# Kernel optimization log

Hardware: AMD Instinct MI355X
Metric: run time of the kernel (lower is better)

## Reference

```python
import jax, jax.numpy as jnp
import numpy as np

N_PIX = 65536
RPT = 16
N_ENT = N_PIX * RPT
DIMS = 128
N_HEADS = 8
LN_EPS = 1e-6


def setup_inputs() -> dict:
    key = jax.random.key(0)
    ks = jax.random.split(key, 12)
    s = 1.0 / np.sqrt(DIMS)
    token = jax.random.normal(ks[0], (N_PIX, DIMS), dtype=jnp.float32)
    ctx = jax.random.normal(ks[1], (N_ENT, DIMS), dtype=jnp.float32)
    segms = jnp.repeat(jnp.arange(N_PIX, dtype=jnp.int32), RPT)  # sorted segment ids
    rpts = jnp.full((N_PIX,), RPT, dtype=jnp.int32)  # sums to N_ENT
    entry_mask = jax.random.bernoulli(ks[2], 0.9, (N_ENT,))
    return {
        "token": token,
        "ctx": ctx,
        "segms": segms,
        "rpts": rpts,
        "entry_mask": entry_mask,
        "Wq": jax.random.normal(ks[3], (DIMS, DIMS), jnp.float32) * s,
        "bq": jnp.zeros((DIMS,), jnp.float32),
        "Wk": jax.random.normal(ks[4], (DIMS, DIMS), jnp.float32) * s,
        "bk": jnp.zeros((DIMS,), jnp.float32),
        "Wv": jax.random.normal(ks[5], (DIMS, DIMS), jnp.float32) * s,
        "bv": jnp.zeros((DIMS,), jnp.float32),
        "Wo": jax.random.normal(ks[6], (DIMS, DIMS), jnp.float32) * s,
        "bo": jnp.zeros((DIMS,), jnp.float32),
        "ln_scale": jnp.ones((DIMS,), jnp.float32),
        "ln_bias": jnp.zeros((DIMS,), jnp.float32),
    }


def reference(token, ctx, segms, rpts, entry_mask,
              Wq, bq, Wk, bk, Wv, bv, Wo, bo, ln_scale, ln_bias):
    EPS = jnp.finfo(jnp.float32).eps
    n_entries = ctx.shape[0]
    n_pixels = token.shape[0]
    dims = ctx.shape[-1]
    hd = dims // N_HEADS  # head dim

    # query per pixel, expanded to entries via ragged repeat
    q = token @ Wq + bq                                          # [P, D]
    q = jnp.repeat(q, rpts, axis=0, total_repeat_length=n_entries)
    q = q.reshape(n_entries, N_HEADS, hd) / jnp.sqrt(jnp.float32(hd))
    k = (ctx @ Wk + bk).reshape(n_entries, N_HEADS, hd)
    v = (ctx @ Wv + bv).reshape(n_entries, N_HEADS, hd)

    w = (q * k).sum(axis=-1, keepdims=True)                      # [E, H, 1]
    off = jax.ops.segment_max(w, segms, num_segments=n_pixels)   # [P, H, 1]
    off = jnp.repeat(off, rpts, axis=0, total_repeat_length=n_entries)
    w = jnp.exp(w - off)
    w = jnp.where(entry_mask[:, None, None], w, 0)
    norm = jax.ops.segment_sum(w, segms, num_segments=n_pixels)
    norm = jnp.repeat(norm, rpts, axis=0, total_repeat_length=n_entries)
    w = w / (norm + EPS)

    res = jax.ops.segment_sum(w * v, segms, num_segments=n_pixels)
    res = res.reshape(n_pixels, dims) @ Wo + bo

    x = token + res
    mu = x.mean(axis=-1, keepdims=True)
    var = ((x - mu) ** 2).mean(axis=-1, keepdims=True)
    y = (x - mu) * jax.lax.rsqrt(var + LN_EPS) * ln_scale + ln_bias
    return y
```

## Files before the change

### kernel.cpp

```cpp
#include <hip/hip_runtime.h>

#define NPIX 65536
#define RPT 16
#define DIMS 128
#define PB 8
#define EB 128
#define TPB 512
#define NBLK 256
#define NTILES (NPIX / PB)
#define TILES_PER_BLK (NTILES / NBLK)
#define LN_EPS 1e-6f
#define SEG_EPS 1.1920928955078125e-07f

typedef __attribute__((ext_vector_type(8))) short bf16x8;
typedef __attribute__((ext_vector_type(4))) short bf16x4;
typedef __attribute__((ext_vector_type(4))) float f32x4;
typedef __attribute__((ext_vector_type(2))) unsigned u32x2;

static __device__ __forceinline__ unsigned pkbf2(float x, float y) {
    unsigned r;
    asm("v_cvt_pk_bf16_f32 %0, %1, %2" : "=v"(r) : "v"(x), "v"(y));
    return r;
}
static __device__ __forceinline__ bf16x4 pk4(float a, float b, float c, float d) {
    u32x2 t; t.x = pkbf2(a, b); t.y = pkbf2(c, d);
    return __builtin_bit_cast(bf16x4, t);
}
static __device__ __forceinline__ unsigned short f2bf(float f) {
    unsigned u = __float_as_uint(f);
    u += 0x7fffu + ((u >> 16) & 1u);
    return (unsigned short)(u >> 16);
}

__global__ void sga_detect_mask(const unsigned* __restrict__ m, int* __restrict__ flag) {
    int lane = threadIdx.x;
    bool not01 = false, notf = false;
    for (int i = 0; i < 16; ++i) {
        unsigned w = m[lane * 16 + i];
        not01 |= (w > 1u);
        notf  |= (w != 0u && w != 0x3F800000u);
    }
    unsigned long long a = __ballot(not01), b = __ballot(notf);
    if (lane == 0) flag[0] = (a == 0ull) ? 0 : ((b == 0ull) ? 1 : 2);
}

__global__ __launch_bounds__(TPB, 2) void sga_kernel(
    const float* __restrict__ token, const float* __restrict__ ctx,
    const unsigned char* __restrict__ emask, const int* __restrict__ mfmt_p,
    const float* __restrict__ Wq, const float* __restrict__ bq,
    const float* __restrict__ Wk, const float* __restrict__ bk,
    const float* __restrict__ Wv, const float* __restrict__ bv,
    const float* __restrict__ Wo, const float* __restrict__ bo,
    const float* __restrict__ lns, const float* __restrict__ lnb,
    float* __restrict__ out)
{
    __shared__ unsigned short s_ctx[2][EB * DIMS];
    __shared__ float          s_x[PB * DIMS];
    __shared__ unsigned short s_tok[PB * DIMS];
    __shared__ unsigned short s_res[PB * DIMS];
    __shared__ unsigned char  s_mask[EB];

    const int tid  = threadIdx.x;
    const int wid  = tid >> 6;
    const int lane = tid & 63;
    const int c    = lane & 15;
    const int g    = lane >> 4;
    const int pc   = c & 7;
    const int nb   = wid * 16;
    const int mfmt = *mfmt_p;
    const f32x4 zf = { 0.f, 0.f, 0.f, 0.f };

    auto stage_mask = [&](size_t ebase) {
        if (tid < EB) {
            unsigned char b;
            if (mfmt == 2)      b = emask[ebase + tid];
            else if (mfmt == 0) b = ((const int*)emask)[ebase + tid] ? 1 : 0;
            else                b = (((const float*)emask)[ebase + tid] != 0.f) ? 1 : 0;
            s_mask[tid] = b;
        }
    };

    bf16x8 wqf[4], wkf[4], wvf[4], wof[4];
    {
        const float* Ws[4] = { Wq, Wk, Wv, Wo };
#pragma unroll
        for (int m = 0; m < 4; ++m) {
#pragma unroll
            for (int ks = 0; ks < 4; ++ks) {
                bf16x8 f;
#pragma unroll
                for (int b = 0; b < 8; ++b) {
                    int kr = ks * 32 + g * 8 + b;
                    f[b] = (short)f2bf(Ws[m][(size_t)kr * DIMS + nb + c]);
                }
                if (m == 0) wqf[ks] = f;
                else if (m == 1) wkf[ks] = f;
                else if (m == 2) wvf[ks] = f;
                else wof[ks] = f;
            }
        }
    }
    const float4 bqv = *(const float4*)(bq + nb + 4 * g);
    const float4 bkv = *(const float4*)(bk + nb + 4 * g);
    const float bv_c = bv[nb + c], bo_c = bo[nb + c];

    const int tile0 = blockIdx.x * TILES_PER_BLK;

    {
        const size_t e0 = (size_t)tile0 * EB;
        float4 v[8]; float4 tv = {0.f,0.f,0.f,0.f};
#pragma unroll
        for (int i = 0; i < 8; ++i) {
            int f4 = i * TPB + tid;
            v[i] = *(const float4*)(ctx + (e0 + (f4 >> 5)) * DIMS + (f4 & 31) * 4);
        }
        if (tid < 256)
            tv = *(const float4*)(token + ((size_t)tile0 * PB + (tid >> 5)) * DIMS + (tid & 31) * 4);
        stage_mask(e0);
#pragma unroll
        for (int i = 0; i < 8; ++i) {
            int f4 = i * TPB + tid; int row = f4 >> 5, colb = (f4 & 31) * 8;
            *(uint2*)((char*)s_ctx[0] + row * 256 + (colb ^ ((row & 7) << 4)))
                = make_uint2(pkbf2(v[i].x, v[i].y), pkbf2(v[i].z, v[i].w));
        }
        if (tid < 256) {
            int row = tid >> 5, colb = (tid & 31) * 8;
            *(uint2*)((char*)s_tok + row * 256 + (colb ^ ((row & 7) << 4)))
                = make_uint2(pkbf2(tv.x, tv.y), pkbf2(tv.z, tv.w));
        }
    }
    __syncthreads();

    for (int t = 0; t < TILES_PER_BLK; ++t) {
        const unsigned short* ctx_c = s_ctx[t & 1];
        unsigned short*       ctx_n = s_ctx[(t & 1) ^ 1];
        const int pb0 = (tile0 + t) * PB;
        const size_t eb1 = (size_t)(pb0 + PB) * RPT;
        const bool pf = (t + 1 < TILES_PER_BLK);

        float4 ca[4], cb[4], tv = {0.f,0.f,0.f,0.f};

        if (pf) {
#pragma unroll
            for (int i = 0; i < 4; ++i) {
                int f4 = i * TPB + tid;
                ca[i] = *(const float4*)(ctx + (eb1 + (f4 >> 5)) * DIMS + (f4 & 31) * 4);
            }
        }

        bf16x4 qb4;
        {
            f32x4 acc = zf;
            int row = pc;
#pragma unroll
            for (int ks = 0; ks < 4; ++ks) {
                int kb = ks * 64 + g * 16;
                bf16x8 a = *(const bf16x8*)((char*)s_tok + row * 256 + (kb ^ ((row & 7) << 4)));
                acc = __builtin_amdgcn_mfma_f32_16x16x32_bf16(wqf[ks], a, acc, 0, 0, 0);
            }
            qb4 = pk4((acc[0] + bqv.x) * 0.25f, (acc[1] + bqv.y) * 0.25f,
                      (acc[2] + bqv.z) * 0.25f, (acc[3] + bqv.w) * 0.25f);
        }

        f32x4 sc = zf;
        bf16x4 vbf[8];
#pragma unroll
        for (int m = 0; m < PB; ++m) {
            f32x4 ak = zf, av = zf;
#pragma unroll
            for (int ks = 0; ks < 4; ++ks) {
                int row = m * 16 + c, kb = ks * 64 + g * 16;
                bf16x8 a = *(const bf16x8*)((const char*)ctx_c + row * 256 + (kb ^ ((row & 7) << 4)));
                ak = __builtin_amdgcn_mfma_f32_16x16x32_bf16(wkf[ks], a, ak, 0, 0, 0);
                av = __builtin_amdgcn_mfma_f32_16x16x32_bf16(a, wvf[ks], av, 0, 0, 0);
            }
            bf16x4 kb4 = pk4(ak[0] + bkv.x, ak[1] + bkv.y, ak[2] + bkv.z, ak[3] + bkv.w);
            vbf[m] = pk4(av[0] + bv_c, av[1] + bv_c, av[2] + bv_c, av[3] + bv_c);
            f32x4 d = __builtin_amdgcn_mfma_f32_16x16x16bf16_1k(kb4, qb4, zf, 0, 0, 0);
#pragma unroll
            for (int r = 0; r < 4; ++r) sc[r] = (pc == m) ? d[r] : sc[r];
        }

        if (pf) {
#pragma unroll
            for (int i = 0; i < 4; ++i) {
                int f4 = i * TPB + tid; int row = f4 >> 5, colb = (f4 & 31) * 8;
                *(uint2*)((char*)ctx_n + row * 256 + (colb ^ ((row & 7) << 4)))
                    = make_uint2(pkbf2(ca[i].x, ca[i].y), pkbf2(ca[i].z, ca[i].w));
            }
#pragma unroll
            for (int i = 0; i < 4; ++i) {
                int f4 = (4 + i) * TPB + tid;
                cb[i] = *(const float4*)(ctx + (eb1 + (f4 >> 5)) * DIMS + (f4 & 31) * 4);
            }
            if (tid < 256)
                tv = *(const float4*)(token + ((size_t)(pb0 + PB) + (tid >> 5)) * DIMS + (tid & 31) * 4);
        }

        unsigned pa_lo, pa_hi;
        {
            float mx = fmaxf(fmaxf(sc[0], sc[1]), fmaxf(sc[2], sc[3]));
            mx = fmaxf(mx, __shfl_xor(mx, 16));
            mx = fmaxf(mx, __shfl_xor(mx, 32));
            unsigned mu_ = *(const unsigned*)(s_mask + pc * 16 + g * 4);
            float e0 = (mu_ & 0xffu)       ? __expf(sc[0] - mx) : 0.f;
            float e1 = (mu_ & 0xff00u)     ? __expf(sc[1] - mx) : 0.f;
            float e2 = (mu_ & 0xff0000u)   ? __expf(sc[2] - mx) : 0.f;
            float e3 = (mu_ & 0xff000000u) ? __expf(sc[3] - mx) : 0.f;
            float sm = e0 + e1 + e2 + e3;
            sm += __shfl_xor(sm, 16); sm += __shfl_xor(sm, 32);
            float inv = 1.f / (sm + SEG_EPS);
            pa_lo = pkbf2(e0 * inv, e1 * inv);
            pa_hi = pkbf2(e2 * inv, e3 * inv);
        }

#pragma unroll
        for (int m = 0; m < PB; ++m) {
            int srcl = ((lane & 48) | m) << 2;
            u32x2 pw;
            pw.x = (unsigned)__builtin_amdgcn_ds_bpermute(srcl, (int)pa_lo);
            pw.y = (unsigned)__builtin_amdgcn_ds_bpermute(srcl, (int)pa_hi);
            bf16x4 pam = __builtin_bit_cast(bf16x4, pw);
            f32x4 rr = __builtin_amdgcn_mfma_f32_16x16x16bf16_1k(pam, vbf[m], zf, 0, 0, 0);
            if (lane < 16) {
                int off2 = m * 256 + (((nb + lane) * 2) ^ ((m & 7) << 4));
                *(unsigned short*)((char*)s_res + off2) = f2bf(rr[0]);
            }
        }
        __syncthreads();

        {
            f32x4 acc = zf;
            int row = pc;
#pragma unroll
            for (int ks = 0; ks < 4; ++ks) {
                int kb = ks * 64 + g * 16;
                bf16x8 a = *(const bf16x8*)((char*)s_res + row * 256 + (kb ^ ((row & 7) << 4)));
                acc = __builtin_amdgcn_mfma_f32_16x16x32_bf16(a, wof[ks], acc, 0, 0, 0);
            }
            if (g < 2) {
#pragma unroll
                for (int r = 0; r < 4; ++r) {
                    int prow = g * 4 + r;
                    unsigned short tb = *(const unsigned short*)((char*)s_tok + prow * 256
                                        + ((((nb + c) * 2)) ^ ((prow & 7) << 4)));
                    float tf = __uint_as_float((unsigned)tb << 16);
                    s_x[prow * DIMS + nb + c] = acc[r] + bo_c + tf;
                }
            }
        }
        __syncthreads();

        {
            int row = wid, c0 = lane * 2;
            float2 x = *(const float2*)(s_x + row * DIMS + c0);
            float s = x.x + x.y;
#pragma unroll
            for (int off = 1; off < 64; off <<= 1) s += __shfl_xor(s, off);
            float mu = s * (1.f / DIMS);
            float dx = x.x - mu, dy = x.y - mu;
            float ss = dx * dx + dy * dy;
#pragma unroll
            for (int off = 1; off < 64; off <<= 1) ss += __shfl_xor(ss, off);
            float rstd = rsqrtf(ss * (1.f / DIMS) + LN_EPS);
            float2 sc2 = *(const float2*)(lns + c0);
            float2 bi = *(const float2*)(lnb + c0);
            float2 y;
            y.x = dx * rstd * sc2.x + bi.x;
            y.y = dy * rstd * sc2.y + bi.y;
            *(float2*)(out + (size_t)(pb0 + row) * DIMS + c0) = y;
        }

        if (pf) {
#pragma unroll
            for (int i = 0; i < 4; ++i) {
                int f4 = (4 + i) * TPB + tid; int row = f4 >> 5, colb = (f4 & 31) * 8;
                *(uint2*)((char*)ctx_n + row * 256 + (colb ^ ((row & 7) << 4)))
                    = make_uint2(pkbf2(cb[i].x, cb[i].y), pkbf2(cb[i].z, cb[i].w));
            }
            if (tid < 256) {
                int row = tid >> 5, colb = (tid & 31) * 8;
                *(uint2*)((char*)s_tok + row * 256 + (colb ^ ((row & 7) << 4)))
                    = make_uint2(pkbf2(tv.x, tv.y), pkbf2(tv.z, tv.w));
            }
            stage_mask(eb1);
        }
        __syncthreads();
    }
}

extern "C" void kernel_launch(void* const* d_in, const int* in_sizes, int n_in,
                              void* d_out, int out_size, void* d_ws, size_t ws_size,
                              hipStream_t stream) {
    const float* token = (const float*)d_in[0];
    const float* ctx   = (const float*)d_in[1];
    const unsigned char* emask = (const unsigned char*)d_in[4];
    const float* Wq = (const float*)d_in[5];  const float* bq = (const float*)d_in[6];
    const float* Wk = (const float*)d_in[7];  const float* bk = (const float*)d_in[8];
    const float* Wv = (const float*)d_in[9];  const float* bv = (const float*)d_in[10];
    const float* Wo = (const float*)d_in[11]; const float* bo = (const float*)d_in[12];
    const float* lns = (const float*)d_in[13]; const float* lnb = (const float*)d_in[14];
    float* out = (float*)d_out;
    int* mfmt = (int*)d_ws;

    sga_detect_mask<<<1, 64, 0, stream>>>((const unsigned*)emask, mfmt);
    sga_kernel<<<NBLK, TPB, 0, stream>>>(token, ctx, emask, mfmt,
                                         Wq, bq, Wk, bk, Wv, bv, Wo, bo,
                                         lns, lnb, out);
}
```

Baseline: 160.3 us.

## Split waves over head pairs and pixel halves to halve LDS ctx reads

```diff
diff --git a/kernel.cpp b/kernel.cpp
--- a/kernel.cpp
+++ b/kernel.cpp
@@ -58,6 +58,7 @@
     __shared__ float          s_x[PB * DIMS];
     __shared__ unsigned short s_tok[PB * DIMS];
     __shared__ unsigned short s_res[PB * DIMS];
+    __shared__ unsigned short s_q[16 * DIMS];
     __shared__ unsigned char  s_mask[EB];
 
     const int tid  = threadIdx.x;
@@ -67,6 +68,10 @@
     const int g    = lane >> 4;
     const int pc   = c & 7;
     const int nb   = wid * 16;
+    const int hp   = wid & 3;
+    const int ph   = wid >> 2;
+    const int nbk0 = hp * 32;
+    const int nbk1 = hp * 32 + 16;
     const int mfmt = *mfmt_p;
     const f32x4 zf = { 0.f, 0.f, 0.f, 0.f };
 
@@ -80,29 +85,29 @@
         }
     };
 
-    bf16x8 wqf[4], wkf[4], wvf[4], wof[4];
-    {
-        const float* Ws[4] = { Wq, Wk, Wv, Wo };
-#pragma unroll
-        for (int m = 0; m < 4; ++m) {
-#pragma unroll
-            for (int ks = 0; ks < 4; ++ks) {
-                bf16x8 f;
-#pragma unroll
-                for (int b = 0; b < 8; ++b) {
-                    int kr = ks * 32 + g * 8 + b;
-                    f[b] = (short)f2bf(Ws[m][(size_t)kr * DIMS + nb + c]);
-                }
-                if (m == 0) wqf[ks] = f;
-                else if (m == 1) wkf[ks] = f;
-                else if (m == 2) wvf[ks] = f;
-                else wof[ks] = f;
-            }
-        }
+    bf16x8 wqf[4], wof[4], wkf[2][4], wvf[2][4];
+#pragma unroll
+    for (int ks = 0; ks < 4; ++ks) {
+        bf16x8 fq, fo, fk0, fk1, fv0, fv1;
+#pragma unroll
+        for (int b = 0; b < 8; ++b) {
+            int kr = ks * 32 + g * 8 + b;
+            fq[b]  = (short)f2bf(Wq[(size_t)kr * DIMS + nb + c]);
+            fo[b]  = (short)f2bf(Wo[(size_t)kr * DIMS + nb + c]);
+            fk0[b] = (short)f2bf(Wk[(size_t)kr * DIMS + nbk0 + c]);
+            fk1[b] = (short)f2bf(Wk[(size_t)kr * DIMS + nbk1 + c]);
+            fv0[b] = (short)f2bf(Wv[(size_t)kr * DIMS + nbk0 + c]);
+            fv1[b] = (short)f2bf(Wv[(size_t)kr * DIMS + nbk1 + c]);
+        }
+        wqf[ks] = fq; wof[ks] = fo;
+        wkf[0][ks] = fk0; wkf[1][ks] = fk1;
+        wvf[0][ks] = fv0; wvf[1][ks] = fv1;
     }
-    const float4 bqv = *(const float4*)(bq + nb + 4 * g);
-    const float4 bkv = *(const float4*)(bk + nb + 4 * g);
-    const float bv_c = bv[nb + c], bo_c = bo[nb + c];
+    const float4 bqv  = *(const float4*)(bq + nb + 4 * g);
+    const float4 bk0v = *(const float4*)(bk + nbk0 + 4 * g);
+    const float4 bk1v = *(const float4*)(bk + nbk1 + 4 * g);
+    const float  bv0  = bv[nbk0 + c], bv1 = bv[nbk1 + c];
+    const float  bo_c = bo[nb + c];
 
     const int tile0 = blockIdx.x * TILES_PER_BLK;
 
@@ -148,7 +153,6 @@
             }
         }
 
-        bf16x4 qb4;
         {
             f32x4 acc = zf;
             int row = pc;
@@ -158,28 +162,43 @@
                 bf16x8 a = *(const bf16x8*)((char*)s_tok + row * 256 + (kb ^ ((row & 7) << 4)));
                 acc = __builtin_amdgcn_mfma_f32_16x16x32_bf16(wqf[ks], a, acc, 0, 0, 0);
             }
-            qb4 = pk4((acc[0] + bqv.x) * 0.25f, (acc[1] + bqv.y) * 0.25f,
-                      (acc[2] + bqv.z) * 0.25f, (acc[3] + bqv.w) * 0.25f);
-        }
-
-        f32x4 sc = zf;
-        bf16x4 vbf[8];
-#pragma unroll
-        for (int m = 0; m < PB; ++m) {
-            f32x4 ak = zf, av = zf;
+            bf16x4 qv = pk4((acc[0] + bqv.x) * 0.25f, (acc[1] + bqv.y) * 0.25f,
+                            (acc[2] + bqv.z) * 0.25f, (acc[3] + bqv.w) * 0.25f);
+            *(bf16x4*)((char*)s_q + c * 256 + (((nb + 4 * g) * 2) ^ ((c & 7) << 4))) = qv;
+        }
+        __syncthreads();
+
+        bf16x4 qb0 = *(const bf16x4*)((char*)s_q + c * 256 + (((nbk0 + 4 * g) * 2) ^ ((c & 7) << 4)));
+        bf16x4 qb1 = *(const bf16x4*)((char*)s_q + c * 256 + (((nbk1 + 4 * g) * 2) ^ ((c & 7) << 4)));
+
+        f32x4 sc0 = zf, sc1 = zf;
+        bf16x4 vb0[4], vb1[4];
+        auto pass1 = [&](int mm) {
+            int m = ph * 4 + mm;
+            f32x4 ak0 = zf, ak1 = zf, av0 = zf, av1 = zf;
 #pragma unroll
             for (int ks = 0; ks < 4; ++ks) {
                 int row = m * 16 + c, kb = ks * 64 + g * 16;
                 bf16x8 a = *(const bf16x8*)((const char*)ctx_c + row * 256 + (kb ^ ((row & 7) << 4)));
-                ak = __builtin_amdgcn_mfma_f32_16x16x32_bf16(wkf[ks], a, ak, 0, 0, 0);
-                av = __builtin_amdgcn_mfma_f32_16x16x32_bf16(a, wvf[ks], av, 0, 0, 0);
-            }
-            bf16x4 kb4 = pk4(ak[0] + bkv.x, ak[1] + bkv.y, ak[2] + bkv.z, ak[3] + bkv.w);
-            vbf[m] = pk4(av[0] + bv_c, av[1] + bv_c, av[2] + bv_c, av[3] + bv_c);
-            f32x4 d = __builtin_amdgcn_mfma_f32_16x16x16bf16_1k(kb4, qb4, zf, 0, 0, 0);
-#pragma unroll
-            for (int r = 0; r < 4; ++r) sc[r] = (pc == m) ? d[r] : sc[r];
-        }
+                ak0 = __builtin_amdgcn_mfma_f32_16x16x32_bf16(wkf[0][ks], a, ak0, 0, 0, 0);
+                av0 = __builtin_amdgcn_mfma_f32_16x16x32_bf16(a, wvf[0][ks], av0, 0, 0, 0);
+                ak1 = __builtin_amdgcn_mfma_f32_16x16x32_bf16(wkf[1][ks], a, ak1, 0, 0, 0);
+                av1 = __builtin_amdgcn_mfma_f32_16x16x32_bf16(a, wvf[1][ks], av1, 0, 0, 0);
+            }
+            bf16x4 kb40 = pk4(ak0[0] + bk0v.x, ak0[1] + bk0v.y, ak0[2] + bk0v.z, ak0[3] + bk0v.w);
+            bf16x4 kb41 = pk4(ak1[0] + bk1v.x, ak1[1] + bk1v.y, ak1[2] + bk1v.z, ak1[3] + bk1v.w);
+            vb0[mm] = pk4(av0[0] + bv0, av0[1] + bv0, av0[2] + bv0, av0[3] + bv0);
+            vb1[mm] = pk4(av1[0] + bv1, av1[1] + bv1, av1[2] + bv1, av1[3] + bv1);
+            f32x4 d0 = __builtin_amdgcn_mfma_f32_16x16x16bf16_1k(kb40, qb0, zf, 0, 0, 0);
+            f32x4 d1 = __builtin_amdgcn_mfma_f32_16x16x16bf16_1k(kb41, qb1, zf, 0, 0, 0);
+#pragma unroll
+            for (int r = 0; r < 4; ++r) {
+                sc0[r] = (pc == m) ? d0[r] : sc0[r];
+                sc1[r] = (pc == m) ? d1[r] : sc1[r];
+            }
+        };
+
+        pass1(0); pass1(1);
 
         if (pf) {
 #pragma unroll
@@ -197,8 +216,9 @@
                 tv = *(const float4*)(token + ((size_t)(pb0 + PB) + (tid >> 5)) * DIMS + (tid & 31) * 4);
         }
 
-        unsigned pa_lo, pa_hi;
-        {
+        pass1(2); pass1(3);
+
+        auto softmax = [&](const f32x4& sc, unsigned& plo, unsigned& phi) {
             float mx = fmaxf(fmaxf(sc[0], sc[1]), fmaxf(sc[2], sc[3]));
             mx = fmaxf(mx, __shfl_xor(mx, 16));
             mx = fmaxf(mx, __shfl_xor(mx, 32));
@@ -210,21 +230,31 @@
             float sm = e0 + e1 + e2 + e3;
             sm += __shfl_xor(sm, 16); sm += __shfl_xor(sm, 32);
             float inv = 1.f / (sm + SEG_EPS);
-            pa_lo = pkbf2(e0 * inv, e1 * inv);
-            pa_hi = pkbf2(e2 * inv, e3 * inv);
-        }
-
-#pragma unroll
-        for (int m = 0; m < PB; ++m) {
+            plo = pkbf2(e0 * inv, e1 * inv);
+            phi = pkbf2(e2 * inv, e3 * inv);
+        };
+        unsigned p0lo, p0hi, p1lo, p1hi;
+        softmax(sc0, p0lo, p0hi);
+        softmax(sc1, p1lo, p1hi);
+
+#pragma unroll
+        for (int mm = 0; mm < 4; ++mm) {
+            int m = ph * 4 + mm;
             int srcl = ((lane & 48) | m) << 2;
-            u32x2 pw;
-            pw.x = (unsigned)__builtin_amdgcn_ds_bpermute(srcl, (int)pa_lo);
-            pw.y = (unsigned)__builtin_amdgcn_ds_bpermute(srcl, (int)pa_hi);
-            bf16x4 pam = __builtin_bit_cast(bf16x4, pw);
-            f32x4 rr = __builtin_amdgcn_mfma_f32_16x16x16bf16_1k(pam, vbf[m], zf, 0, 0, 0);
+            u32x2 pw0, pw1;
+            pw0.x = (unsigned)__builtin_amdgcn_ds_bpermute(srcl, (int)p0lo);
+            pw0.y = (unsigned)__builtin_amdgcn_ds_bpermute(srcl, (int)p0hi);
+            pw1.x = (unsigned)__builtin_amdgcn_ds_bpermute(srcl, (int)p1lo);
+            pw1.y = (unsigned)__builtin_amdgcn_ds_bpermute(srcl, (int)p1hi);
+            bf16x4 pam0 = __builtin_bit_cast(bf16x4, pw0);
+            bf16x4 pam1 = __builtin_bit_cast(bf16x4, pw1);
+            f32x4 rr0 = __builtin_amdgcn_mfma_f32_16x16x16bf16_1k(pam0, vb0[mm], zf, 0, 0, 0);
+            f32x4 rr1 = __builtin_amdgcn_mfma_f32_16x16x16bf16_1k(pam1, vb1[mm], zf, 0, 0, 0);
             if (lane < 16) {
-                int off2 = m * 256 + (((nb + lane) * 2) ^ ((m & 7) << 4));
-                *(unsigned short*)((char*)s_res + off2) = f2bf(rr[0]);
+                int o0 = m * 256 + (((nbk0 + lane) * 2) ^ ((m & 7) << 4));
+                int o1 = m * 256 + (((nbk1 + lane) * 2) ^ ((m & 7) << 4));
+                *(unsigned short*)((char*)s_res + o0) = f2bf(rr0[0]);
+                *(unsigned short*)((char*)s_res + o1) = f2bf(rr1[0]);
             }
         }
         __syncthreads();
```

Measured after the change: 248.4 us. +54.9%, slower.
